# Kernel optimization log

Measured on AMD Instinct MI355X. Metric: run time of the kernel, lower is better.

## Reference

```python
import jax, jax.numpy as jnp
import numpy as np

BN_EPS = 1e-5


def spmm(rows, cols, vals, x):
    # Sparse [V,V] @ x for x: [B, V, F]. COO (rows, cols, vals) with E nnz.
    B, V, F = x.shape
    xt = jnp.transpose(x, (1, 0, 2)).reshape(V, B * F)      # [V, B*F]
    msg = xt[cols] * vals[:, None]                           # [E, B*F]
    y = jax.ops.segment_sum(msg, rows, num_segments=V)       # [V, B*F]
    return jnp.transpose(y.reshape(V, B, F), (1, 0, 2))      # [B, V, F]


def cheb_conv(rows, cols, vals, x, W, b):
    # Chebyshev graph conv: out = sum_k T_k(L) x @ W[k] + b ; W: [K, Fin, Fout]
    K = W.shape[0]
    x0 = x
    out = jnp.einsum('bvi,io->bvo', x0, W[0])
    if K > 1:
        x1 = spmm(rows, cols, vals, x0)
        out = out + jnp.einsum('bvi,io->bvo', x1, W[1])
        for k in range(2, K):
            x2 = 2.0 * spmm(rows, cols, vals, x1) - x0
            out = out + jnp.einsum('bvi,io->bvo', x2, W[k])
            x0, x1 = x1, x2
    return out + b


def bn_relu(x, gamma, beta):
    # BatchNorm1d (training stats) over (batch, nodes) per channel, then ReLU.
    m = jnp.mean(x, axis=(0, 1))
    v = jnp.var(x, axis=(0, 1))
    y = (x - m) * jax.lax.rsqrt(v + BN_EPS) * gamma + beta
    return jax.nn.relu(y)


def setup_inputs() -> dict:
    key = jax.random.key(0)
    ks = jax.random.split(key, 8)
    V, DEG, B, CIN, COUT = 49152, 20, 2, 128, 64
    x = jax.random.normal(ks[0], (B, V, CIN), dtype=jnp.float32)
    # HEALPix-like sparse Laplacian: diagonal + 20 random neighbors per node
    self_idx = jnp.arange(V, dtype=jnp.int32)
    nbr = jax.random.randint(ks[1], (V * DEG,), 0, V, dtype=jnp.int32)
    rows = jnp.concatenate([self_idx, jnp.repeat(self_idx, DEG)])
    cols = jnp.concatenate([self_idx, nbr])
    vals = jax.random.normal(ks[2], (V * (DEG + 1),), dtype=jnp.float32) * 0.1
    def w(k, shape):
        fan_in = shape[0] * shape[1]
        return jax.random.normal(k, shape, dtype=jnp.float32) * np.float32(np.sqrt(2.0 / fan_in))
    return {
        'x': x, 'rows': rows, 'cols': cols, 'vals': vals,
        'W1': w(ks[3], (1, CIN, COUT)), 'b1': jnp.zeros((COUT,), jnp.float32),
        'g1': jnp.ones((COUT,), jnp.float32), 'be1': jnp.zeros((COUT,), jnp.float32),
        'W2': w(ks[4], (3, COUT, COUT)), 'b2': jnp.zeros((COUT,), jnp.float32),
        'g2': jnp.ones((COUT,), jnp.float32), 'be2': jnp.zeros((COUT,), jnp.float32),
        'W3': w(ks[5], (1, COUT, CIN)), 'b3': jnp.zeros((CIN,), jnp.float32),
        'g3': jnp.ones((CIN,), jnp.float32), 'be3': jnp.zeros((CIN,), jnp.float32),
    }


def reference(x, rows, cols, vals, W1, b1, g1, be1, W2, b2, g2, be2, W3, b3, g3, be3):
    h = bn_relu(cheb_conv(rows, cols, vals, x, W1, b1), g1, be1)   # [B,V,64]
    h = bn_relu(cheb_conv(rows, cols, vals, h, W2, b2), g2, be2)   # [B,V,64]
    h = bn_relu(cheb_conv(rows, cols, vals, h, W3, b3), g3, be3)   # [B,V,128]
    return h
```

## Files before the change

kernel.cpp:

```cpp
#include <hip/hip_runtime.h>

#define VN 49152
#define DEG 20
#define NB 2
#define MROWS (NB * VN)

static constexpr float BN_EPS = 1e-5f;

typedef short bf16x8 __attribute__((ext_vector_type(8)));
typedef float floatx4 __attribute__((ext_vector_type(4)));

__device__ __forceinline__ unsigned short f2bf(float f) {
  unsigned int u = __builtin_bit_cast(unsigned int, f);
  u += 0x7FFFu + ((u >> 16) & 1u);
  return (unsigned short)(u >> 16);
}
__device__ __forceinline__ float bf2f(unsigned short h) {
  unsigned int u = ((unsigned int)h) << 16;
  return __builtin_bit_cast(float, u);
}
__device__ __forceinline__ float bflo(unsigned int u) {
  return __builtin_bit_cast(float, u << 16);
}
__device__ __forceinline__ float bfhi(unsigned int u) {
  return __builtin_bit_cast(float, u & 0xFFFF0000u);
}
__device__ __forceinline__ unsigned int packbf(float a, float b) {
  return (unsigned int)f2bf(a) | ((unsigned int)f2bf(b) << 16);
}

__device__ __forceinline__ void scsh_from8(const float* __restrict__ g,
    int RS, int c, int S, const float* __restrict__ gamma,
    const float* __restrict__ beta, float& sc, float& sh) {
  float s = 0.f, s2 = 0.f;
  #pragma unroll
  for (int r = 0; r < 8; ++r) { s += g[r * RS + c]; s2 += g[r * RS + S + c]; }
  float mean = s * (1.f / MROWS);
  float var  = s2 * (1.f / MROWS) - mean * mean;
  sc = gamma[c] * rsqrtf(var + BN_EPS);
  sh = beta[c] - mean * sc;
}

#define TRS 72

#define LDA1 136
__global__ __launch_bounds__(256) void gemm1(const float* __restrict__ X,
    const float* __restrict__ W, const float* __restrict__ bias,
    unsigned short* __restrict__ Y, float* __restrict__ gsum) {
  __shared__ unsigned short As[128 * LDA1];
  __shared__ unsigned short Bs[64 * LDA1];
  __shared__ float sred[128];
  int t = threadIdx.x;
  int row0 = blockIdx.x * 128;
  if (t < 128) sred[t] = 0.f;
  const float* Xt = X + (size_t)row0 * 128;
  #pragma unroll
  for (int c = 0; c < 16; ++c) {
    int f4i = c * 256 + t;
    int row = f4i >> 5, k = (f4i & 31) * 4;
    float4 v = *(const float4*)(Xt + row * 128 + k);
    *(uint2*)(&As[row * LDA1 + k]) = make_uint2(packbf(v.x, v.y), packbf(v.z, v.w));
  }
  #pragma unroll
  for (int c = 0; c < 32; ++c) {
    int f = c * 256 + t;
    int k = f >> 6, n = f & 63;
    Bs[n * LDA1 + k] = f2bf(W[f]);
  }
  __syncthreads();
  int l = t & 63, wv = t >> 6;
  int lr = l & 15, q = l >> 4;
  int m0 = wv * 32;
  floatx4 acc[2][4];
  #pragma unroll
  for (int mi = 0; mi < 2; ++mi)
    #pragma unroll
    for (int ni = 0; ni < 4; ++ni) acc[mi][ni] = (floatx4)(0.f);
  #pragma unroll
  for (int ks = 0; ks < 128; ks += 32) {
    bf16x8 af[2], bfr[4];
    #pragma unroll
    for (int mi = 0; mi < 2; ++mi)
      af[mi] = *(const bf16x8*)(&As[(m0 + mi * 16 + lr) * LDA1 + ks + q * 8]);
    #pragma unroll
    for (int ni = 0; ni < 4; ++ni)
      bfr[ni] = *(const bf16x8*)(&Bs[(ni * 16 + lr) * LDA1 + ks + q * 8]);
    #pragma unroll
    for (int mi = 0; mi < 2; ++mi)
      #pragma unroll
      for (int ni = 0; ni < 4; ++ni)
        acc[mi][ni] = __builtin_amdgcn_mfma_f32_16x16x32_bf16(af[mi], bfr[ni], acc[mi][ni], 0, 0, 0);
  }
  __syncthreads();
  int b = (row0 >= VN) ? 1 : 0;
  int b2 = b * 2, vb0 = row0 - b * VN;
  #pragma unroll
  for (int ni = 0; ni < 4; ++ni) {
    int col = ni * 16 + lr;
    float bv = bias[col];
    float s = 0.f, s2 = 0.f;
    #pragma unroll
    for (int mi = 0; mi < 2; ++mi)
      #pragma unroll
      for (int r = 0; r < 4; ++r) {
        float y = acc[mi][ni][r] + bv;
        s += y; s2 += y * y;
        As[(m0 + mi * 16 + q * 4 + r) * TRS + col] = f2bf(y);
      }
    atomicAdd(&sred[col], s);
    atomicAdd(&sred[64 + col], s2);
  }
  __syncthreads();
  #pragma unroll
  for (int i = 0; i < 4; ++i) {
    int idx = i * 256 + t;
    int p = idx >> 9, rem = idx & 511;
    int rowIdx = rem >> 2, ch0 = (rem & 3) * 8;
    uint4 d = *(const uint4*)(&As[rowIdx * TRS + p * 32 + ch0]);
    *(uint4*)(Y + ((size_t)(b2 + p) * VN + vb0 + rowIdx) * 32 + ch0) = d;
  }
  if (t < 128) atomicAdd(&gsum[(blockIdx.x & 7) * 128 + t], sred[t]);
}

__global__ __launch_bounds__(256) void spmm1(const unsigned short* __restrict__ T1,
    const int* __restrict__ cols, const float* __restrict__ vals,
    const float* __restrict__ gsum, const float* __restrict__ gamma,
    const float* __restrict__ beta, unsigned short* __restrict__ X1out) {
  __shared__ float scsh_s[64];
  int g = blockIdx.x;
  int combo = (g & 7) >> 1;
  int rg = ((g >> 3) << 1) | (g & 1);
  int t = threadIdx.x;
  int cwin0 = (combo & 1) * 32;
  if (t < 32) {
    float sc, sh;
    scsh_from8(gsum, 128, cwin0 + t, 64, gamma, beta, sc, sh);
    scsh_s[t] = sc; scsh_s[32 + t] = sh;
  }
  __syncthreads();
  int wv = t >> 6, lane = t & 63;
  int v = rg * 64 + wv * 16 + (lane >> 2);
  int ch0 = (lane & 3) * 8;
  float sc[8], sh[8];
  #pragma unroll
  for (int j = 0; j < 8; ++j) { sc[j] = scsh_s[ch0 + j]; sh[j] = scsh_s[32 + ch0 + j]; }
  const unsigned short* __restrict__ plane = T1 + (size_t)combo * VN * 32;
  float a[8];
  {
    float w0 = vals[v];
    uint4 d = *(const uint4*)(plane + (size_t)v * 32 + ch0);
    float e[8] = {bflo(d.x), bfhi(d.x), bflo(d.y), bfhi(d.y),
                  bflo(d.z), bfhi(d.z), bflo(d.w), bfhi(d.w)};
    #pragma unroll
    for (int j = 0; j < 8; ++j) {
      float h = fmaf(e[j], sc[j], sh[j]);
      h = h > 0.f ? h : 0.f;
      a[j] = w0 * h;
    }
  }
  const int*   __restrict__ cp = cols + VN + v * DEG;
  const float* __restrict__ vp = vals + VN + v * DEG;
  #pragma unroll
  for (int j = 0; j < DEG; ++j) {
    int cj = cp[j];
    float wj = vp[j];
    uint4 d = *(const uint4*)(plane + (size_t)cj * 32 + ch0);
    float e[8] = {bflo(d.x), bfhi(d.x), bflo(d.y), bfhi(d.y),
                  bflo(d.z), bfhi(d.z), bflo(d.w), bfhi(d.w)};
    #pragma unroll
    for (int i = 0; i < 8; ++i) {
      float h = fmaf(e[i], sc[i], sh[i]);
      h = h > 0.f ? h : 0.f;
      a[i] = fmaf(h, wj, a[i]);
    }
  }
  uint4 o;
  o.x = packbf(a[0], a[1]); o.y = packbf(a[2], a[3]);
  o.z = packbf(a[4], a[5]); o.w = packbf(a[6], a[7]);
  *(uint4*)(X1out + (size_t)combo * VN * 32 + (size_t)v * 32 + ch0) = o;
}

__global__ __launch_bounds__(256) void spmm2(const unsigned short* __restrict__ X1,
    const unsigned short* __restrict__ T1, const int* __restrict__ cols,
    const float* __restrict__ vals, const float* __restrict__ gsum,
    const float* __restrict__ gamma, const float* __restrict__ beta,
    unsigned short* __restrict__ X2out) {
  __shared__ float scsh_s[64];
  int g = blockIdx.x;
  int combo = (g & 7) >> 1;
  int rg = ((g >> 3) << 1) | (g & 1);
  int t = threadIdx.x;
  int cwin0 = (combo & 1) * 32;
  if (t < 32) {
    float sc, sh;
    scsh_from8(gsum, 128, cwin0 + t, 64, gamma, beta, sc, sh);
    scsh_s[t] = sc; scsh_s[32 + t] = sh;
  }
  __syncthreads();
  int wv = t >> 6, lane = t & 63;
  int v = rg * 64 + wv * 16 + (lane >> 2);
  int ch0 = (lane & 3) * 8;
  const size_t pbase = (size_t)combo * VN * 32;
  const size_t myoff = pbase + (size_t)v * 32 + ch0;
  const unsigned short* __restrict__ plane = X1 + pbase;
  float a[8];
  {
    float w0 = vals[v];
    uint4 d = *(const uint4*)(X1 + myoff);
    a[0] = w0 * bflo(d.x); a[1] = w0 * bfhi(d.x);
    a[2] = w0 * bflo(d.y); a[3] = w0 * bfhi(d.y);
    a[4] = w0 * bflo(d.z); a[5] = w0 * bfhi(d.z);
    a[6] = w0 * bflo(d.w); a[7] = w0 * bfhi(d.w);
  }
  const int*   __restrict__ cp = cols + VN + v * DEG;
  const float* __restrict__ vp = vals + VN + v * DEG;
  #pragma unroll
  for (int j = 0; j < DEG; ++j) {
    int cj = cp[j];
    float wj = vp[j];
    uint4 d = *(const uint4*)(plane + (size_t)cj * 32 + ch0);
    a[0] = fmaf(bflo(d.x), wj, a[0]); a[1] = fmaf(bfhi(d.x), wj, a[1]);
    a[2] = fmaf(bflo(d.y), wj, a[2]); a[3] = fmaf(bfhi(d.y), wj, a[3]);
    a[4] = fmaf(bflo(d.z), wj, a[4]); a[5] = fmaf(bfhi(d.z), wj, a[5]);
    a[6] = fmaf(bflo(d.w), wj, a[6]); a[7] = fmaf(bfhi(d.w), wj, a[7]);
  }
  float sc[8], sh[8];
  #pragma unroll
  for (int j = 0; j < 8; ++j) { sc[j] = scsh_s[ch0 + j]; sh[j] = scsh_s[32 + ch0 + j]; }
  uint4 hr = *(const uint4*)(T1 + myoff);
  float e[8] = {bflo(hr.x), bfhi(hr.x), bflo(hr.y), bfhi(hr.y),
                bflo(hr.z), bfhi(hr.z), bflo(hr.w), bfhi(hr.w)};
  float oo[8];
  #pragma unroll
  for (int j = 0; j < 8; ++j) {
    float h = fmaf(e[j], sc[j], sh[j]);
    h = h > 0.f ? h : 0.f;
    oo[j] = 2.f * a[j] - h;
  }
  uint4 o;
  o.x = packbf(oo[0], oo[1]); o.y = packbf(oo[2], oo[3]);
  o.z = packbf(oo[4], oo[5]); o.w = packbf(oo[6], oo[7]);
  *(uint4*)(X2out + myoff) = o;
}

#define LDA2 72
__global__ __launch_bounds__(256) void gemm2(const unsigned short* X0,
    const unsigned short* __restrict__ X1, const unsigned short* __restrict__ X2,
    const float* __restrict__ W, const float* __restrict__ bias,
    const float* __restrict__ gsumIn, const float* __restrict__ gamma,
    const float* __restrict__ beta, unsigned short* Y,
    float* __restrict__ gsumOut) {
  __shared__ unsigned short As[128 * LDA2];
  __shared__ unsigned short Bs[64 * LDA2];
  __shared__ float sred[128];
  __shared__ float scsh_s[128];
  int t = threadIdx.x;
  int row0 = blockIdx.x * 128;
  int b = (row0 >= VN) ? 1 : 0;
  int b2 = b * 2;
  int vb0 = row0 - b * VN;
  if (t < 128) sred[t] = 0.f;
  if (t >= 128 && t < 192) {
    int c = t - 128;
    float sc, sh;
    scsh_from8(gsumIn, 128, c, 64, gamma, beta, sc, sh);
    scsh_s[c] = sc; scsh_s[64 + c] = sh;
  }
  __syncthreads();
  int kk = (t & 15) * 4;
  int r0 = t >> 4;
  float tsc[4], tsh[4];
  #pragma unroll
  for (int j = 0; j < 4; ++j) { tsc[j] = scsh_s[kk + j]; tsh[j] = scsh_s[64 + kk + j]; }
  int l = t & 63, wv = t >> 6;
  int lr = l & 15, q = l >> 4;
  int m0 = wv * 32;
  floatx4 acc[2][4];
  #pragma unroll
  for (int mi = 0; mi < 2; ++mi)
    #pragma unroll
    for (int ni = 0; ni < 4; ++ni) acc[mi][ni] = (floatx4)(0.f);

  #pragma unroll
  for (int term = 0; term < 3; ++term) {
    const unsigned short* Xp = (term == 0) ? X0 : (term == 1) ? X1 : X2;
    const float* Wt = W + term * 64 * 64;
    const unsigned short* srcBase =
        Xp + ((size_t)(b2 + (kk >> 5)) * VN + vb0) * 32 + (kk & 31);
    #pragma unroll
    for (int c8 = 0; c8 < 8; ++c8) {
      int row = c8 * 16 + r0;
      uint2 rawv = *(const uint2*)(srcBase + (size_t)row * 32);
      if (term == 0) {
        float y0 = fmaf(bflo(rawv.x), tsc[0], tsh[0]);
        float y1 = fmaf(bfhi(rawv.x), tsc[1], tsh[1]);
        float y2 = fmaf(bflo(rawv.y), tsc[2], tsh[2]);
        float y3 = fmaf(bfhi(rawv.y), tsc[3], tsh[3]);
        y0 = y0 > 0.f ? y0 : 0.f; y1 = y1 > 0.f ? y1 : 0.f;
        y2 = y2 > 0.f ? y2 : 0.f; y3 = y3 > 0.f ? y3 : 0.f;
        *(uint2*)(&As[row * LDA2 + kk]) = make_uint2(packbf(y0, y1), packbf(y2, y3));
      } else {
        *(uint2*)(&As[row * LDA2 + kk]) = rawv;
      }
    }
    #pragma unroll
    for (int c = 0; c < 16; ++c) {
      int f = c * 256 + t;
      int k = f >> 6, n = f & 63;
      Bs[n * LDA2 + k] = f2bf(Wt[f]);
    }
    __syncthreads();
    #pragma unroll
    for (int ks = 0; ks < 64; ks += 32) {
      bf16x8 af[2], bfr[4];
      #pragma unroll
      for (int mi = 0; mi < 2; ++mi)
        af[mi] = *(const bf16x8*)(&As[(m0 + mi * 16 + lr) * LDA2 + ks + q * 8]);
      #pragma unroll
      for (int ni = 0; ni < 4; ++ni)
        bfr[ni] = *(const bf16x8*)(&Bs[(ni * 16 + lr) * LDA2 + ks + q * 8]);
      #pragma unroll
      for (int mi = 0; mi < 2; ++mi)
        #pragma unroll
        for (int ni = 0; ni < 4; ++ni)
          acc[mi][ni] = __builtin_amdgcn_mfma_f32_16x16x32_bf16(af[mi], bfr[ni], acc[mi][ni], 0, 0, 0);
    }
    __syncthreads();
  }
  #pragma unroll
  for (int ni = 0; ni < 4; ++ni) {
    int col = ni * 16 + lr;
    float bv = bias[col];
    float s = 0.f, s2 = 0.f;
    #pragma unroll
    for (int mi = 0; mi < 2; ++mi)
      #pragma unroll
      for (int r = 0; r < 4; ++r) {
        float y = acc[mi][ni][r] + bv;
        s += y; s2 += y * y;
        As[(m0 + mi * 16 + q * 4 + r) * TRS + col] = f2bf(y);
      }
    atomicAdd(&sred[col], s);
    atomicAdd(&sred[64 + col], s2);
  }
  __syncthreads();
  #pragma unroll
  for (int i = 0; i < 4; ++i) {
    int idx = i * 256 + t;
    int p = idx >> 9, rem = idx & 511;
    int rowIdx = rem >> 2, ch0 = (rem & 3) * 8;
    uint4 d = *(const uint4*)(&As[rowIdx * TRS + p * 32 + ch0]);
    *(uint4*)(Y + ((size_t)(b2 + p) * VN + vb0 + rowIdx) * 32 + ch0) = d;
  }
  if (t < 128) atomicAdd(&gsumOut[(blockIdx.x & 7) * 128 + t], sred[t]);
}

__global__ __launch_bounds__(256) void gemm3(const unsigned short* __restrict__ X,
    const float* __restrict__ W, const float* __restrict__ bias,
    const float* __restrict__ gsumIn, const float* __restrict__ gamma,
    const float* __restrict__ beta, unsigned short* __restrict__ Y,
    float* __restrict__ gsumOut) {
  __shared__ unsigned short As[128 * LDA2];
  __shared__ unsigned short Bs[64 * LDA2];
  __shared__ float sred[128];
  __shared__ float scsh_s[128];
  int t = threadIdx.x;
  int row0 = blockIdx.x * 128;
  int n0 = blockIdx.y * 64;
  int b = (row0 >= VN) ? 1 : 0;
  int b2 = b * 2;
  int vb0 = row0 - b * VN;
  if (t < 128) sred[t] = 0.f;
  if (t >= 128 && t < 192) {
    int c = t - 128;
    float sc, sh;
    scsh_from8(gsumIn, 128, c, 64, gamma, beta, sc, sh);
    scsh_s[c] = sc; scsh_s[64 + c] = sh;
  }
  __syncthreads();
  int kk = (t & 15) * 4;
  int r0 = t >> 4;
  float tsc[4], tsh[4];
  #pragma unroll
  for (int j = 0; j < 4; ++j) { tsc[j] = scsh_s[kk + j]; tsh[j] = scsh_s[64 + kk + j]; }
  const unsigned short* srcBase =
      X + ((size_t)(b2 + (kk >> 5)) * VN + vb0) * 32 + (kk & 31);
  #pragma unroll
  for (int c8 = 0; c8 < 8; ++c8) {
    int row = c8 * 16 + r0;
    uint2 rawv = *(const uint2*)(srcBase + (size_t)row * 32);
    float y0 = fmaf(bflo(rawv.x), tsc[0], tsh[0]);
    float y1 = fmaf(bfhi(rawv.x), tsc[1], tsh[1]);
    float y2 = fmaf(bflo(rawv.y), tsc[2], tsh[2]);
    float y3 = fmaf(bfhi(rawv.y), tsc[3], tsh[3]);
    y0 = y0 > 0.f ? y0 : 0.f; y1 = y1 > 0.f ? y1 : 0.f;
    y2 = y2 > 0.f ? y2 : 0.f; y3 = y3 > 0.f ? y3 : 0.f;
    *(uint2*)(&As[row * LDA2 + kk]) = make_uint2(packbf(y0, y1), packbf(y2, y3));
  }
  #pragma unroll
  for (int c = 0; c < 16; ++c) {
    int f = c * 256 + t;
    int k = f >> 6, n = f & 63;
    Bs[n * LDA2 + k] = f2bf(W[k * 128 + n0 + n]);
  }
  __syncthreads();
  int l = t & 63, wv = t >> 6;
  int lr = l & 15, q = l >> 4;
  int m0 = wv * 32;
  floatx4 acc[2][4];
  #pragma unroll
  for (int mi = 0; mi < 2; ++mi)
    #pragma unroll
    for (int ni = 0; ni < 4; ++ni) acc[mi][ni] = (floatx4)(0.f);
  #pragma unroll
  for (int ks = 0; ks < 64; ks += 32) {
    bf16x8 af[2], bfr[4];
    #pragma unroll
    for (int mi = 0; mi < 2; ++mi)
      af[mi] = *(const bf16x8*)(&As[(m0 + mi * 16 + lr) * LDA2 + ks + q * 8]);
    #pragma unroll
    for (int ni = 0; ni < 4; ++ni)
      bfr[ni] = *(const bf16x8*)(&Bs[(ni * 16 + lr) * LDA2 + ks + q * 8]);
    #pragma unroll
    for (int mi = 0; mi < 2; ++mi)
      #pragma unroll
      for (int ni = 0; ni < 4; ++ni)
        acc[mi][ni] = __builtin_amdgcn_mfma_f32_16x16x32_bf16(af[mi], bfr[ni], acc[mi][ni], 0, 0, 0);
  }
  __syncthreads();
  #pragma unroll
  for (int ni = 0; ni < 4; ++ni) {
    int lc = ni * 16 + lr;
    int col = n0 + lc;
    float bv = bias[col];
    float s = 0.f, s2 = 0.f;
    #pragma unroll
    for (int mi = 0; mi < 2; ++mi)
      #pragma unroll
      for (int r = 0; r < 4; ++r) {
        float y = acc[mi][ni][r] + bv;
        s += y; s2 += y * y;
        As[(m0 + mi * 16 + q * 4 + r) * TRS + lc] = f2bf(y);
      }
    atomicAdd(&sred[lc], s);
    atomicAdd(&sred[64 + lc], s2);
  }
  __syncthreads();
  #pragma unroll
  for (int i = 0; i < 4; ++i) {
    int idx = i * 256 + t;
    int rowIdx = idx >> 3, c0 = (idx & 7) * 8;
    uint4 d = *(const uint4*)(&As[rowIdx * TRS + c0]);
    *(uint4*)(Y + (size_t)(row0 + rowIdx) * 128 + n0 + c0) = d;
  }
  if (t < 128) {
    int lc = t & 63, p = t >> 6;
    atomicAdd(&gsumOut[(blockIdx.x & 7) * 256 + p * 128 + n0 + lc], sred[t]);
  }
}

__global__ __launch_bounds__(256) void bn_apply_final(const unsigned short* __restrict__ T,
    float* __restrict__ Y, const float* __restrict__ gsum,
    const float* __restrict__ gamma, const float* __restrict__ beta) {
  __shared__ float scsh_s[256];
  int t = threadIdx.x;
  if (t < 128) {
    float sc, sh;
    scsh_from8(gsum, 256, t, 128, gamma, beta, sc, sh);
    scsh_s[t] = sc; scsh_s[128 + t] = sh;
  }
  __syncthreads();
  size_t i4 = ((size_t)blockIdx.x * 256 + t) * 4;
  int c0 = (int)(i4 & 127);
  ushort4 tv = *(const ushort4*)(T + i4);
  unsigned short sv[4] = {tv.x, tv.y, tv.z, tv.w};
  float ov[4];
  #pragma unroll
  for (int j = 0; j < 4; ++j) {
    int c = c0 + j;
    float y = fmaf(bf2f(sv[j]), scsh_s[c], scsh_s[128 + c]);
    ov[j] = y > 0.f ? y : 0.f;
  }
  *(float4*)(Y + i4) = make_float4(ov[0], ov[1], ov[2], ov[3]);
}

extern "C" void kernel_launch(void* const* d_in, const int* in_sizes, int n_in,
                              void* d_out, int out_size, void* d_ws, size_t ws_size,
                              hipStream_t stream) {
  const float* x    = (const float*)d_in[0];
  const int*   cols = (const int*)  d_in[2];
  const float* vals = (const float*)d_in[3];
  const float* W1   = (const float*)d_in[4];
  const float* b1   = (const float*)d_in[5];
  const float* g1   = (const float*)d_in[6];
  const float* be1  = (const float*)d_in[7];
  const float* W2   = (const float*)d_in[8];
  const float* b2   = (const float*)d_in[9];
  const float* g2   = (const float*)d_in[10];
  const float* be2  = (const float*)d_in[11];
  const float* W3   = (const float*)d_in[12];
  const float* b3   = (const float*)d_in[13];
  const float* g3   = (const float*)d_in[14];
  const float* be3  = (const float*)d_in[15];
  float* out = (float*)d_out;

  const size_t PL = (size_t)MROWS * 64;
  unsigned short* P0 = (unsigned short*)d_ws;
  unsigned short* P1 = P0 + PL;
  unsigned short* P2 = P1 + PL;
  float* ctrl  = (float*)(P2 + 2 * PL);
  float* gsum1 = ctrl;
  float* gsum2 = ctrl + 1024;
  float* gsum3 = ctrl + 2048;

  hipMemsetAsync(ctrl, 0, 4096 * sizeof(float), stream);

  dim3 blk(256);
  int rowb = MROWS / 128;
  int spmm_blocks = 3072;
  int ap128_blocks = (int)(PL * 2 / 4 / 256);

  gemm1<<<rowb, blk, 0, stream>>>(x, W1, b1, P0, gsum1);

  spmm1<<<spmm_blocks, blk, 0, stream>>>(P0, cols, vals, gsum1, g1, be1, P1);
  spmm2<<<spmm_blocks, blk, 0, stream>>>(P1, P0, cols, vals, gsum1, g1, be1, P2);
  gemm2<<<rowb, blk, 0, stream>>>(P0, P1, P2, W2, b2, gsum1, g1, be1, P0, gsum2);

  dim3 g3grid(rowb, 2);
  gemm3<<<g3grid, blk, 0, stream>>>(P0, W3, b3, gsum2, g2, be2, P2, gsum3);
  bn_apply_final<<<ap128_blocks, blk, 0, stream>>>(P2, out, gsum3, g3, be3);
}
```

Before: 259.2 us.

## Fold Chebyshev recurrence into weights and double-buffer A tiles in gemm2

The second SpMM pass now writes only Z = L·x1, with no read of T1 and no BN/ReLU recompute. The recurrence x2 = 2Z − x0 is folded into the weights as W0−W2, W1 and 2·W2. gemm2 preloads all three converted weight tiles into shared memory up front. It also prefetches the next A operand into registers while MFMAs run on the current buffer, using two A buffers. Folding the subtraction into the weights changes bf16 rounding slightly and uses more shared memory per block, which may lower occupancy.

```diff
diff --git a/kernel.cpp b/kernel.cpp
--- a/kernel.cpp
+++ b/kernel.cpp
@@ -180,23 +180,13 @@
   *(uint4*)(X1out + (size_t)combo * VN * 32 + (size_t)v * 32 + ch0) = o;
 }
 
-__global__ __launch_bounds__(256) void spmm2(const unsigned short* __restrict__ X1,
-    const unsigned short* __restrict__ T1, const int* __restrict__ cols,
-    const float* __restrict__ vals, const float* __restrict__ gsum,
-    const float* __restrict__ gamma, const float* __restrict__ beta,
-    unsigned short* __restrict__ X2out) {
-  __shared__ float scsh_s[64];
+__global__ __launch_bounds__(256) void spmmz(const unsigned short* __restrict__ X1,
+    const int* __restrict__ cols, const float* __restrict__ vals,
+    unsigned short* __restrict__ Zout) {
   int g = blockIdx.x;
   int combo = (g & 7) >> 1;
   int rg = ((g >> 3) << 1) | (g & 1);
   int t = threadIdx.x;
-  int cwin0 = (combo & 1) * 32;
-  if (t < 32) {
-    float sc, sh;
-    scsh_from8(gsum, 128, cwin0 + t, 64, gamma, beta, sc, sh);
-    scsh_s[t] = sc; scsh_s[32 + t] = sh;
-  }
-  __syncthreads();
   int wv = t >> 6, lane = t & 63;
   int v = rg * 64 + wv * 16 + (lane >> 2);
   int ch0 = (lane & 3) * 8;
@@ -224,34 +214,21 @@
     a[4] = fmaf(bflo(d.z), wj, a[4]); a[5] = fmaf(bfhi(d.z), wj, a[5]);
     a[6] = fmaf(bflo(d.w), wj, a[6]); a[7] = fmaf(bfhi(d.w), wj, a[7]);
   }
-  float sc[8], sh[8];
-  #pragma unroll
-  for (int j = 0; j < 8; ++j) { sc[j] = scsh_s[ch0 + j]; sh[j] = scsh_s[32 + ch0 + j]; }
-  uint4 hr = *(const uint4*)(T1 + myoff);
-  float e[8] = {bflo(hr.x), bfhi(hr.x), bflo(hr.y), bfhi(hr.y),
-                bflo(hr.z), bfhi(hr.z), bflo(hr.w), bfhi(hr.w)};
-  float oo[8];
-  #pragma unroll
-  for (int j = 0; j < 8; ++j) {
-    float h = fmaf(e[j], sc[j], sh[j]);
-    h = h > 0.f ? h : 0.f;
-    oo[j] = 2.f * a[j] - h;
-  }
   uint4 o;
-  o.x = packbf(oo[0], oo[1]); o.y = packbf(oo[2], oo[3]);
-  o.z = packbf(oo[4], oo[5]); o.w = packbf(oo[6], oo[7]);
-  *(uint4*)(X2out + myoff) = o;
+  o.x = packbf(a[0], a[1]); o.y = packbf(a[2], a[3]);
+  o.z = packbf(a[4], a[5]); o.w = packbf(a[6], a[7]);
+  *(uint4*)(Zout + myoff) = o;
 }
 
 #define LDA2 72
 __global__ __launch_bounds__(256) void gemm2(const unsigned short* X0,
-    const unsigned short* __restrict__ X1, const unsigned short* __restrict__ X2,
+    const unsigned short* __restrict__ X1, const unsigned short* __restrict__ Z,
     const float* __restrict__ W, const float* __restrict__ bias,
     const float* __restrict__ gsumIn, const float* __restrict__ gamma,
     const float* __restrict__ beta, unsigned short* Y,
     float* __restrict__ gsumOut) {
-  __shared__ unsigned short As[128 * LDA2];
-  __shared__ unsigned short Bs[64 * LDA2];
+  __shared__ unsigned short As[2][128 * LDA2];
+  __shared__ unsigned short Bs[3][64 * LDA2];
   __shared__ float sred[128];
   __shared__ float scsh_s[128];
   int t = threadIdx.x;
@@ -266,12 +243,18 @@
     scsh_from8(gsumIn, 128, c, 64, gamma, beta, sc, sh);
     scsh_s[c] = sc; scsh_s[64 + c] = sh;
   }
+  #pragma unroll
+  for (int c = 0; c < 16; ++c) {
+    int f = c * 256 + t;
+    int k = f >> 6, n = f & 63;
+    float w0 = W[f], w1 = W[4096 + f], w2 = W[8192 + f];
+    Bs[0][n * LDA2 + k] = f2bf(w0 - w2);
+    Bs[1][n * LDA2 + k] = f2bf(w1);
+    Bs[2][n * LDA2 + k] = f2bf(2.f * w2);
+  }
   __syncthreads();
   int kk = (t & 15) * 4;
   int r0 = t >> 4;
-  float tsc[4], tsh[4];
-  #pragma unroll
-  for (int j = 0; j < 4; ++j) { tsc[j] = scsh_s[kk + j]; tsh[j] = scsh_s[64 + kk + j]; }
   int l = t & 63, wv = t >> 6;
   int lr = l & 15, q = l >> 4;
   int m0 = wv * 32;
@@ -281,52 +264,76 @@
     #pragma unroll
     for (int ni = 0; ni < 4; ++ni) acc[mi][ni] = (floatx4)(0.f);
 
-  #pragma unroll
-  for (int term = 0; term < 3; ++term) {
-    const unsigned short* Xp = (term == 0) ? X0 : (term == 1) ? X1 : X2;
-    const float* Wt = W + term * 64 * 64;
-    const unsigned short* srcBase =
-        Xp + ((size_t)(b2 + (kk >> 5)) * VN + vb0) * 32 + (kk & 31);
+  {
+    float tsc[4], tsh[4];
+    #pragma unroll
+    for (int j = 0; j < 4; ++j) { tsc[j] = scsh_s[kk + j]; tsh[j] = scsh_s[64 + kk + j]; }
+    const unsigned short* src0 =
+        X0 + ((size_t)(b2 + (kk >> 5)) * VN + vb0) * 32 + (kk & 31);
     #pragma unroll
     for (int c8 = 0; c8 < 8; ++c8) {
       int row = c8 * 16 + r0;
-      uint2 rawv = *(const uint2*)(srcBase + (size_t)row * 32);
-      if (term == 0) {
-        float y0 = fmaf(bflo(rawv.x), tsc[0], tsh[0]);
-        float y1 = fmaf(bfhi(rawv.x), tsc[1], tsh[1]);
-        float y2 = fmaf(bflo(rawv.y), tsc[2], tsh[2]);
-        float y3 = fmaf(bfhi(rawv.y), tsc[3], tsh[3]);
-        y0 = y0 > 0.f ? y0 : 0.f; y1 = y1 > 0.f ? y1 : 0.f;
-        y2 = y2 > 0.f ? y2 : 0.f; y3 = y3 > 0.f ? y3 : 0.f;
-        *(uint2*)(&As[row * LDA2 + kk]) = make_uint2(packbf(y0, y1), packbf(y2, y3));
-      } else {
-        *(uint2*)(&As[row * LDA2 + kk]) = rawv;
-      }
+      uint2 rawv = *(const uint2*)(src0 + (size_t)row * 32);
+      float y0 = fmaf(bflo(rawv.x), tsc[0], tsh[0]);
+      float y1 = fmaf(bfhi(rawv.x), tsc[1], tsh[1]);
+      float y2 = fmaf(bflo(rawv.y), tsc[2], tsh[2]);
+      float y3 = fmaf(bfhi(rawv.y), tsc[3], tsh[3]);
+      y0 = y0 > 0.f ? y0 : 0.f; y1 = y1 > 0.f ? y1 : 0.f;
+      y2 = y2 > 0.f ? y2 : 0.f; y3 = y3 > 0.f ? y3 : 0.f;
+      *(uint2*)(&As[0][row * LDA2 + kk]) = make_uint2(packbf(y0, y1), packbf(y2, y3));
     }
-    #pragma unroll
-    for (int c = 0; c < 16; ++c) {
-      int f = c * 256 + t;
-      int k = f >> 6, n = f & 63;
-      Bs[n * LDA2 + k] = f2bf(Wt[f]);
-    }
-    __syncthreads();
-    #pragma unroll
-    for (int ks = 0; ks < 64; ks += 32) {
-      bf16x8 af[2], bfr[4];
-      #pragma unroll
-      for (int mi = 0; mi < 2; ++mi)
-        af[mi] = *(const bf16x8*)(&As[(m0 + mi * 16 + lr) * LDA2 + ks + q * 8]);
-      #pragma unroll
-      for (int ni = 0; ni < 4; ++ni)
-        bfr[ni] = *(const bf16x8*)(&Bs[(ni * 16 + lr) * LDA2 + ks + q * 8]);
-      #pragma unroll
-      for (int mi = 0; mi < 2; ++mi)
-        #pragma unroll
-        for (int ni = 0; ni < 4; ++ni)
-          acc[mi][ni] = __builtin_amdgcn_mfma_f32_16x16x32_bf16(af[mi], bfr[ni], acc[mi][ni], 0, 0, 0);
-    }
-    __syncthreads();
-  }
+  }
+  __syncthreads();
+
+#define MFMA_TERM(AS, BIDX)                                                     \
+  {                                                                             \
+    _Pragma("unroll")                                                           \
+    for (int ks = 0; ks < 64; ks += 32) {                                       \
+      bf16x8 af[2], bfr[4];                                                     \
+      _Pragma("unroll")                                                         \
+      for (int mi = 0; mi < 2; ++mi)                                            \
+        af[mi] = *(const bf16x8*)(&AS[(m0 + mi * 16 + lr) * LDA2 + ks + q * 8]);\
+      _Pragma("unroll")                                                         \
+      for (int ni = 0; ni < 4; ++ni)                                            \
+        bfr[ni] = *(const bf16x8*)(&Bs[BIDX][(ni * 16 + lr) * LDA2 + ks + q * 8]);\
+      _Pragma("unroll")                                                         \
+      for (int mi = 0; mi < 2; ++mi)                                            \
+        _Pragma("unroll")                                                       \
+        for (int ni = 0; ni < 4; ++ni)                                          \
+          acc[mi][ni] = __builtin_amdgcn_mfma_f32_16x16x32_bf16(af[mi], bfr[ni],\
+                                                          acc[mi][ni], 0, 0, 0);\
+    }                                                                           \
+  }
+
+  uint2 pf[8];
+  {
+    const unsigned short* src1 =
+        X1 + ((size_t)(b2 + (kk >> 5)) * VN + vb0) * 32 + (kk & 31);
+    #pragma unroll
+    for (int c8 = 0; c8 < 8; ++c8)
+      pf[c8] = *(const uint2*)(src1 + (size_t)(c8 * 16 + r0) * 32);
+    MFMA_TERM(As[0], 0);
+    #pragma unroll
+    for (int c8 = 0; c8 < 8; ++c8)
+      *(uint2*)(&As[1][(c8 * 16 + r0) * LDA2 + kk]) = pf[c8];
+  }
+  __syncthreads();
+  {
+    const unsigned short* src2 =
+        Z + ((size_t)(b2 + (kk >> 5)) * VN + vb0) * 32 + (kk & 31);
+    #pragma unroll
+    for (int c8 = 0; c8 < 8; ++c8)
+      pf[c8] = *(const uint2*)(src2 + (size_t)(c8 * 16 + r0) * 32);
+    MFMA_TERM(As[1], 1);
+    #pragma unroll
+    for (int c8 = 0; c8 < 8; ++c8)
+      *(uint2*)(&As[0][(c8 * 16 + r0) * LDA2 + kk]) = pf[c8];
+  }
+  __syncthreads();
+  MFMA_TERM(As[0], 2);
+  __syncthreads();
+#undef MFMA_TERM
+
   #pragma unroll
   for (int ni = 0; ni < 4; ++ni) {
     int col = ni * 16 + lr;
@@ -338,7 +345,7 @@
       for (int r = 0; r < 4; ++r) {
         float y = acc[mi][ni][r] + bv;
         s += y; s2 += y * y;
-        As[(m0 + mi * 16 + q * 4 + r) * TRS + col] = f2bf(y);
+        As[0][(m0 + mi * 16 + q * 4 + r) * TRS + col] = f2bf(y);
       }
     atomicAdd(&sred[col], s);
     atomicAdd(&sred[64 + col], s2);
@@ -349,7 +356,7 @@
     int idx = i * 256 + t;
     int p = idx >> 9, rem = idx & 511;
     int rowIdx = rem >> 2, ch0 = (rem & 3) * 8;
-    uint4 d = *(const uint4*)(&As[rowIdx * TRS + p * 32 + ch0]);
+    uint4 d = *(const uint4*)(&As[0][rowIdx * TRS + p * 32 + ch0]);
     *(uint4*)(Y + ((size_t)(b2 + p) * VN + vb0 + rowIdx) * 32 + ch0) = d;
   }
   if (t < 128) atomicAdd(&gsumOut[(blockIdx.x & 7) * 128 + t], sred[t]);
@@ -523,7 +530,7 @@
   gemm1<<<rowb, blk, 0, stream>>>(x, W1, b1, P0, gsum1);
 
   spmm1<<<spmm_blocks, blk, 0, stream>>>(P0, cols, vals, gsum1, g1, be1, P1);
-  spmm2<<<spmm_blocks, blk, 0, stream>>>(P1, P0, cols, vals, gsum1, g1, be1, P2);
+  spmmz<<<spmm_blocks, blk, 0, stream>>>(P1, cols, vals, P2);
   gemm2<<<rowb, blk, 0, stream>>>(P0, P1, P2, W2, b2, gsum1, g1, be1, P0, gsum2);
 
   dim3 g3grid(rowb, 2);
```

New measurement: 263.8 us. Within noise of the previous version (+1.8%).
